# Optimization experiments

Hardware: AMD Instinct MI355X
Metric: run time of the kernel (lower is better)

The kernel has to match this reference:

```python
import jax, jax.numpy as jnp
import numpy as np

N = 50000        # nodes
E = 800000       # edges
IN_FEAT = 128
OUT_FEAT = 64
HEADS = 4
NUM_CLASSES = 40
NEG_SLOPE = 0.2  # DGL GATConv default


def setup_inputs() -> dict:
    key = jax.random.key(0)
    ks = jax.random.split(key, 12)
    x = jax.random.normal(ks[0], (N, IN_FEAT), dtype=jnp.float32)
    src = jax.random.randint(ks[1], (E,), 0, N, dtype=jnp.int32)
    dst = jax.random.randint(ks[2], (E,), 0, N, dtype=jnp.int32)
    # layer 1 params: fc W1 [in, H*D], attn_l/attn_r [H, D], bias [H*D]
    s1 = 1.0 / np.sqrt(IN_FEAT)
    W1 = jax.random.normal(ks[3], (IN_FEAT, HEADS * OUT_FEAT), dtype=jnp.float32) * s1
    al1 = jax.random.normal(ks[4], (HEADS, OUT_FEAT), dtype=jnp.float32) * 0.1
    ar1 = jax.random.normal(ks[5], (HEADS, OUT_FEAT), dtype=jnp.float32) * 0.1
    b1 = jnp.zeros((HEADS * OUT_FEAT,), dtype=jnp.float32)
    # layer 2 params: fc W2 [H*D, C], attn [1, C], bias [C]
    hid = HEADS * OUT_FEAT
    s2 = 1.0 / np.sqrt(hid)
    W2 = jax.random.normal(ks[6], (hid, NUM_CLASSES), dtype=jnp.float32) * s2
    al2 = jax.random.normal(ks[7], (1, NUM_CLASSES), dtype=jnp.float32) * 0.1
    ar2 = jax.random.normal(ks[8], (1, NUM_CLASSES), dtype=jnp.float32) * 0.1
    b2 = jnp.zeros((NUM_CLASSES,), dtype=jnp.float32)
    return {"x": x, "src": src, "dst": dst,
            "W1": W1, "al1": al1, "ar1": ar1, "b1": b1,
            "W2": W2, "al2": al2, "ar2": ar2, "b2": b2}


def gat_layer(x, W, al, ar, bias, src, dst, heads, out_feat):
    n = x.shape[0]
    h = (x @ W).reshape(n, heads, out_feat)            # [N,H,D]
    el = jnp.sum(h * al[None], axis=-1)                # [N,H]
    er = jnp.sum(h * ar[None], axis=-1)                # [N,H]
    e = el[src] + er[dst]                              # [E,H]
    e = jnp.where(e > 0, e, NEG_SLOPE * e)             # LeakyReLU
    # segment softmax over edges sharing the same destination
    emax = jax.ops.segment_max(e, dst, num_segments=n)           # [N,H]
    emax = jnp.where(jnp.isfinite(emax), emax, 0.0)              # isolated nodes
    ee = jnp.exp(e - emax[dst])                                  # [E,H]
    denom = jax.ops.segment_sum(ee, dst, num_segments=n)         # [N,H]
    denom = jnp.where(denom > 0, denom, 1.0)
    alpha = ee / denom[dst]                                      # [E,H]
    msg = h[src] * alpha[:, :, None]                             # [E,H,D]
    out = jax.ops.segment_sum(msg, dst, num_segments=n)          # [N,H,D]
    return out + bias.reshape(1, heads, out_feat)


def reference(x, src, dst, W1, al1, ar1, b1, W2, al2, ar2, b2):
    h = gat_layer(x, W1, al1, ar1, b1, src, dst, HEADS, OUT_FEAT)  # [N,H,D]
    h = h.reshape(h.shape[0], HEADS * OUT_FEAT)
    h = jax.nn.elu(h)
    h = gat_layer(h, W2, al2, ar2, b2, src, dst, 1, NUM_CLASSES)   # [N,1,C]
    return jnp.squeeze(h, axis=1)                                   # [N,C]
```

## Files before the change

### kernel.cpp

```cpp
#include <hip/hip_runtime.h>

#define NN 50000
#define NE 800000
#define HID 256
#define NCLS 40

typedef short bf16x8 __attribute__((ext_vector_type(8)));
typedef float f32x4 __attribute__((ext_vector_type(4)));

__device__ inline unsigned short f2bf(float f) {
    unsigned int u = __float_as_uint(f);
    return (unsigned short)((u + 0x7FFFu + ((u >> 16) & 1u)) >> 16);
}
__device__ inline unsigned int pack2bf(float a, float b) {
    return (unsigned int)f2bf(a) | ((unsigned int)f2bf(b) << 16);
}
__device__ inline float2 bf2x(unsigned int u) {
    return make_float2(__uint_as_float(u << 16), __uint_as_float(u & 0xFFFF0000u));
}

__global__ void k_count(const int* __restrict__ dst, int* __restrict__ counts) {
    int e = blockIdx.x * 256 + threadIdx.x;
    if (e < NE) atomicAdd(&counts[dst[e]], 1);
}

__global__ void k_scanA(const int* __restrict__ counts, int* __restrict__ indptr,
                        int* __restrict__ bsum) {
    __shared__ int sh[256];
    int t = threadIdx.x;
    int idx = blockIdx.x * 256 + t;
    int c = idx < NN ? counts[idx] : 0;
    sh[t] = c;
    __syncthreads();
    for (int off = 1; off < 256; off <<= 1) {
        int v = (t >= off) ? sh[t - off] : 0;
        __syncthreads();
        sh[t] += v;
        __syncthreads();
    }
    if (idx < NN) indptr[idx] = sh[t] - c;
    if (t == 255) bsum[blockIdx.x] = sh[255];
}

__global__ void k_scanB(int* __restrict__ bsum, int nb) {
    __shared__ int sh[256];
    int t = threadIdx.x;
    int c = t < nb ? bsum[t] : 0;
    sh[t] = c;
    __syncthreads();
    for (int off = 1; off < 256; off <<= 1) {
        int v = (t >= off) ? sh[t - off] : 0;
        __syncthreads();
        sh[t] += v;
        __syncthreads();
    }
    if (t < nb) bsum[t] = sh[t] - c;
}

__global__ void k_scanC(int* __restrict__ indptr, const int* __restrict__ bsum,
                        int* __restrict__ fill) {
    int idx = blockIdx.x * 256 + threadIdx.x;
    if (idx < NN) {
        indptr[idx] += bsum[idx >> 8];
        fill[idx] = 0;
    }
    if (idx == 0) indptr[NN] = NE;
}

__global__ void k_scatter(const int* __restrict__ src, const int* __restrict__ dst,
                          const int* __restrict__ indptr, int* __restrict__ fill,
                          int* __restrict__ srcs) {
    int e = blockIdx.x * 256 + threadIdx.x;
    if (e < NE) {
        int d = dst[e];
        int pos = atomicAdd(&fill[d], 1);
        srcs[indptr[d] + pos] = src[e];
    }
}

__global__ void k_prep(const float* __restrict__ W1, const float* __restrict__ al,
                       const float* __restrict__ ar, const float* __restrict__ W2,
                       float* __restrict__ wel, float* __restrict__ wer,
                       unsigned short* __restrict__ W1Tb,
                       unsigned short* __restrict__ W2Tb) {
    int gid = blockIdx.x * 256 + threadIdx.x;
    int nth = gridDim.x * 256;
    const int TOT = 512 + 32768 + 48 * 256;
    for (int i = gid; i < TOT; i += nth) {
        if (i < 512) {
            int k = i >> 2, h = i & 3;
            float a = 0.f, b = 0.f;
            for (int dd = 0; dd < 64; ++dd) {
                float w = W1[k * 256 + h * 64 + dd];
                a = fmaf(w, al[h * 64 + dd], a);
                b = fmaf(w, ar[h * 64 + dd], b);
            }
            wel[i] = a;
            wer[i] = b;
        } else if (i < 512 + 32768) {
            int j = i - 512;
            int col = j >> 7, k = j & 127;
            W1Tb[j] = f2bf(W1[k * 256 + col]);
        } else {
            int j = i - 512 - 32768;
            int col = j >> 8, kk = j & 255;
            W2Tb[j] = (col < NCLS) ? f2bf(W2[kk * 40 + col]) : (unsigned short)0;
        }
    }
}

__global__ void k_elr1x(const float* __restrict__ x, const float* __restrict__ wel,
                        const float* __restrict__ wer, float* __restrict__ el1,
                        float* __restrict__ er1, unsigned short* __restrict__ xb) {
    __shared__ float xs[64 * 129];
    __shared__ float wels[512], wers[512];
    int t = threadIdx.x;
    int n0 = blockIdx.x * 64;
    wels[t] = wel[t]; wels[256 + t] = wel[256 + t];
    wers[t] = wer[t]; wers[256 + t] = wer[256 + t];
    for (int i = 0; i < 8; ++i) {
        int f = i * 256 + t;
        int row = f >> 5;
        int col4 = (f & 31) * 4;
        float4 v = make_float4(0.f, 0.f, 0.f, 0.f);
        if (n0 + row < NN) v = ((const float4*)x)[(size_t)n0 * 32 + f];
        xs[row * 129 + col4 + 0] = v.x;
        xs[row * 129 + col4 + 1] = v.y;
        xs[row * 129 + col4 + 2] = v.z;
        xs[row * 129 + col4 + 3] = v.w;
    }
    __syncthreads();
    int node = t & 63;
    int h = t >> 6;
    float a = 0.f, b = 0.f;
    for (int k = 0; k < 128; ++k) {
        float xv = xs[node * 129 + k];
        a = fmaf(xv, wels[k * 4 + h], a);
        b = fmaf(xv, wers[k * 4 + h], b);
    }
    if (n0 + node < NN) {
        el1[(size_t)(n0 + node) * 4 + h] = a;
        er1[(size_t)(n0 + node) * 4 + h] = b;
    }
    for (int i = 0; i < 4; ++i) {
        int g = (i * 256 + t) * 8;
        int row = g >> 7, col = g & 127;
        if (n0 + row < NN) {
            ushort4 lo, hi;
            lo.x = f2bf(xs[row * 129 + col + 0]);
            lo.y = f2bf(xs[row * 129 + col + 1]);
            lo.z = f2bf(xs[row * 129 + col + 2]);
            lo.w = f2bf(xs[row * 129 + col + 3]);
            hi.x = f2bf(xs[row * 129 + col + 4]);
            hi.y = f2bf(xs[row * 129 + col + 5]);
            hi.z = f2bf(xs[row * 129 + col + 6]);
            hi.w = f2bf(xs[row * 129 + col + 7]);
            *(ushort4*)&xb[(size_t)(n0 + row) * 128 + col] = lo;
            *(ushort4*)&xb[(size_t)(n0 + row) * 128 + col + 4] = hi;
        }
    }
}

#define XG_STRIDE 260
__global__ void k_agg1m(const unsigned int* __restrict__ xb32,
                        const float* __restrict__ el1, const float* __restrict__ er1,
                        const int* __restrict__ indptr, const int* __restrict__ srcs,
                        const unsigned short* __restrict__ W1Tb,
                        const float* __restrict__ b1,
                        unsigned short* __restrict__ elu1) {
    __shared__ unsigned int xg[16 * XG_STRIDE];
    __shared__ int   si[4][64];
    __shared__ float4 sw[4][64];
    int t = threadIdx.x;
    int wv = t >> 6, l = t & 63;
    int n0 = blockIdx.x * 16;
    int d0 = n0 + wv * 4;
    int ip[5];
#pragma unroll
    for (int q = 0; q < 5; ++q) ip[q] = indptr[d0 + q];
    int s_next = 0;
    float4 ls_next = make_float4(0.f, 0.f, 0.f, 0.f);
    {
        int deg0 = ip[1] - ip[0];
        if (l < deg0) {
            s_next = srcs[ip[0] + l];
            ls_next = *(const float4*)&el1[(size_t)s_next * 4];
        }
    }
    for (int rr = 0; rr < 4; ++rr) {
        int d = d0 + rr;
        int beg = ip[rr], end = ip[rr + 1];
        int deg = end - beg;
        float4 rd = *(const float4*)&er1[(size_t)d * 4];
        int s_l = s_next;
        float4 ls = ls_next;
        float4 w = make_float4(0.f, 0.f, 0.f, 0.f);
        if (l < deg) {
            float e0 = ls.x + rd.x, e1 = ls.y + rd.y, e2 = ls.z + rd.z, e3 = ls.w + rd.w;
            e0 = e0 > 0.f ? e0 : 0.2f * e0;
            e1 = e1 > 0.f ? e1 : 0.2f * e1;
            e2 = e2 > 0.f ? e2 : 0.2f * e2;
            e3 = e3 > 0.f ? e3 : 0.2f * e3;
            w = make_float4(__expf(e0), __expf(e1), __expf(e2), __expf(e3));
        }
        si[wv][l] = s_l;
        sw[wv][l] = w;
        if (rr < 3) {
            int degn = ip[rr + 2] - ip[rr + 1];
            s_next = 0;
            ls_next = make_float4(0.f, 0.f, 0.f, 0.f);
            if (l < degn) {
                s_next = srcs[ip[rr + 1] + l];
                ls_next = *(const float4*)&el1[(size_t)s_next * 4];
            }
        }
        float2 a0 = {0.f, 0.f}, a1 = {0.f, 0.f}, a2 = {0.f, 0.f}, a3 = {0.f, 0.f};
        int dege = deg < 64 ? deg : 64;
        for (int e = 0; e < dege; e += 8) {
            int ixs[8];
            float4 wss[8];
            unsigned int us[8];
#pragma unroll
            for (int q = 0; q < 8; ++q) {
                ixs[q] = si[wv][e + q];
                wss[q] = sw[wv][e + q];
            }
#pragma unroll
            for (int q = 0; q < 8; ++q) us[q] = xb32[(size_t)ixs[q] * 64 + l];
#pragma unroll
            for (int q = 0; q < 8; ++q) {
                float2 xv = bf2x(us[q]);
                float4 wq = wss[q];
                a0.x = fmaf(wq.x, xv.x, a0.x); a0.y = fmaf(wq.x, xv.y, a0.y);
                a1.x = fmaf(wq.y, xv.x, a1.x); a1.y = fmaf(wq.y, xv.y, a1.y);
                a2.x = fmaf(wq.z, xv.x, a2.x); a2.y = fmaf(wq.z, xv.y, a2.y);
                a3.x = fmaf(wq.w, xv.x, a3.x); a3.y = fmaf(wq.w, xv.y, a3.y);
            }
        }
        float s0 = w.x, s1 = w.y, s2 = w.z, s3 = w.w;
        for (int j = beg + 64 + l; j < end; j += 64) {
            float4 lsx = *(const float4*)&el1[(size_t)srcs[j] * 4];
            float e0 = lsx.x + rd.x, e1 = lsx.y + rd.y, e2 = lsx.z + rd.z, e3 = lsx.w + rd.w;
            e0 = e0 > 0.f ? e0 : 0.2f * e0;
            e1 = e1 > 0.f ? e1 : 0.2f * e1;
            e2 = e2 > 0.f ? e2 : 0.2f * e2;
            e3 = e3 > 0.f ? e3 : 0.2f * e3;
            s0 += __expf(e0); s1 += __expf(e1); s2 += __expf(e2); s3 += __expf(e3);
        }
        for (int j = beg + 64; j < end; ++j) {
            int s = srcs[j];
            float4 lsx = *(const float4*)&el1[(size_t)s * 4];
            float e0 = lsx.x + rd.x, e1 = lsx.y + rd.y, e2 = lsx.z + rd.z, e3 = lsx.w + rd.w;
            e0 = e0 > 0.f ? e0 : 0.2f * e0;
            e1 = e1 > 0.f ? e1 : 0.2f * e1;
            e2 = e2 > 0.f ? e2 : 0.2f * e2;
            e3 = e3 > 0.f ? e3 : 0.2f * e3;
            float w0 = __expf(e0), w1 = __expf(e1), w2 = __expf(e2), w3 = __expf(e3);
            float2 xv = bf2x(xb32[(size_t)s * 64 + l]);
            a0.x = fmaf(w0, xv.x, a0.x); a0.y = fmaf(w0, xv.y, a0.y);
            a1.x = fmaf(w1, xv.x, a1.x); a1.y = fmaf(w1, xv.y, a1.y);
            a2.x = fmaf(w2, xv.x, a2.x); a2.y = fmaf(w2, xv.y, a2.y);
            a3.x = fmaf(w3, xv.x, a3.x); a3.y = fmaf(w3, xv.y, a3.y);
        }
#pragma unroll
        for (int off = 32; off > 0; off >>= 1) {
            s0 += __shfl_xor(s0, off);
            s1 += __shfl_xor(s1, off);
            s2 += __shfl_xor(s2, off);
            s3 += __shfl_xor(s3, off);
        }
        float i0 = s0 > 0.f ? 1.f / s0 : 0.f;
        float i1 = s1 > 0.f ? 1.f / s1 : 0.f;
        float i2 = s2 > 0.f ? 1.f / s2 : 0.f;
        float i3 = s3 > 0.f ? 1.f / s3 : 0.f;
        unsigned int* xgn = &xg[(wv * 4 + rr) * XG_STRIDE];
        xgn[0 * 64 + l] = pack2bf(a0.x * i0, a0.y * i0);
        xgn[1 * 64 + l] = pack2bf(a1.x * i1, a1.y * i1);
        xgn[2 * 64 + l] = pack2bf(a2.x * i2, a2.y * i2);
        xgn[3 * 64 + l] = pack2bf(a3.x * i3, a3.y * i3);
    }
    __syncthreads();
    int lrow = l & 15, lk = l >> 4;
    f32x4 acc[4] = {};
#pragma unroll
    for (int kt = 0; kt < 4; ++kt) {
        bf16x8 av = *(const bf16x8*)&xg[lrow * XG_STRIDE + wv * 64 + kt * 16 + lk * 4];
#pragma unroll
        for (int nt = 0; nt < 4; ++nt) {
            int col = wv * 64 + nt * 16 + lrow;
            bf16x8 bv = *(const bf16x8*)&W1Tb[(size_t)col * 128 + kt * 32 + lk * 8];
            acc[nt] = __builtin_amdgcn_mfma_f32_16x16x32_bf16(av, bv, acc[nt], 0, 0, 0);
        }
    }
#pragma unroll
    for (int nt = 0; nt < 4; ++nt) {
        int col = wv * 64 + nt * 16 + lrow;
        float bv1 = b1[col];
#pragma unroll
        for (int r = 0; r < 4; ++r) {
            int row = n0 + lk * 4 + r;
            float o = acc[nt][r] + bv1;
            o = o > 0.f ? o : (__expf(o) - 1.f);
            elu1[(size_t)row * 256 + col] = f2bf(o);
        }
    }
}

__global__ void k_mfma2(const unsigned short* __restrict__ elu1,
                        const unsigned short* __restrict__ W2Tb,
                        const float* __restrict__ al2, const float* __restrict__ ar2,
                        unsigned short* __restrict__ h2b, float* __restrict__ el2,
                        float* __restrict__ er2) {
    int t = threadIdx.x;
    int wv = t >> 6, l = t & 63;
    int lrow = l & 15, lk = l >> 4;
    int n0 = blockIdx.x * 64 + wv * 16;
    int arow = n0 + lrow;
    if (arow >= NN) arow = NN - 1;
    f32x4 acc[3] = {};
#pragma unroll
    for (int kt = 0; kt < 8; ++kt) {
        int kofs = kt * 32 + lk * 8;
        bf16x8 av = *(const bf16x8*)&elu1[(size_t)arow * 256 + kofs];
#pragma unroll
        for (int nt = 0; nt < 3; ++nt) {
            bf16x8 bv = *(const bf16x8*)&W2Tb[(size_t)(nt * 16 + lrow) * 256 + kofs];
            acc[nt] = __builtin_amdgcn_mfma_f32_16x16x32_bf16(av, bv, acc[nt], 0, 0, 0);
        }
    }
    float alc[3], arc[3];
#pragma unroll
    for (int nt = 0; nt < 3; ++nt) {
        int col = nt * 16 + lrow;
        alc[nt] = col < NCLS ? al2[col] : 0.f;
        arc[nt] = col < NCLS ? ar2[col] : 0.f;
    }
#pragma unroll
    for (int r = 0; r < 4; ++r) {
        int row = n0 + lk * 4 + r;
        float pa = 0.f, pb = 0.f;
#pragma unroll
        for (int nt = 0; nt < 3; ++nt) {
            float v = acc[nt][r];
            pa = fmaf(v, alc[nt], pa);
            pb = fmaf(v, arc[nt], pb);
            int col = nt * 16 + lrow;
            if (row < NN && col < NCLS) h2b[(size_t)row * NCLS + col] = f2bf(v);
        }
#pragma unroll
        for (int off = 1; off < 16; off <<= 1) {
            pa += __shfl_xor(pa, off);
            pb += __shfl_xor(pb, off);
        }
        if (lrow == 0 && row < NN) {
            el2[row] = pa;
            er2[row] = pb;
        }
    }
}

__global__ void k_agg2(const unsigned int* __restrict__ h2b32,
                       const float* __restrict__ el2,
                       const float* __restrict__ er2, const float* __restrict__ b2,
                       const int* __restrict__ indptr, const int* __restrict__ srcs,
                       float* __restrict__ out) {
    __shared__ int   si[4][64];
    __shared__ float sw[4][64];
    int t = threadIdx.x;
    int wv = t >> 6, l = t & 63;
    int d = blockIdx.x * 4 + wv;
    int beg = indptr[d], end = indptr[d + 1];
    int deg = end - beg;
    float rd = er2[d];
    int s_l = 0;
    float w = 0.f;
    if (l < deg) {
        s_l = srcs[beg + l];
        float e = el2[s_l] + rd;
        e = e > 0.f ? e : 0.2f * e;
        w = __expf(e);
    }
    si[wv][l] = s_l;
    sw[wv][l] = w;
    float den = w;
    for (int j = beg + 64 + l; j < end; j += 64) {
        float e = el2[srcs[j]] + rd;
        e = e > 0.f ? e : 0.2f * e;
        den += __expf(e);
    }
    int half = l >> 5, il = l & 31;
    bool act = il < 20;
    float2 acc = {0.f, 0.f};
    int dege = deg < 64 ? deg : 64;
    for (int e = 0; e < dege; e += 8) {
        int ixs[4];
        float ws_[4];
        unsigned int us[4];
#pragma unroll
        for (int q = 0; q < 4; ++q) {
            int idx = e + 2 * q + half;
            ixs[q] = si[wv][idx];
            ws_[q] = sw[wv][idx];
        }
#pragma unroll
        for (int q = 0; q < 4; ++q)
            us[q] = act ? h2b32[(size_t)ixs[q] * 20 + il] : 0u;
#pragma unroll
        for (int q = 0; q < 4; ++q) {
            float2 xv = bf2x(us[q]);
            acc.x = fmaf(ws_[q], xv.x, acc.x);
            acc.y = fmaf(ws_[q], xv.y, acc.y);
        }
    }
    for (int j = beg + 64; j < end; ++j) {
        int s = srcs[j];
        float e = el2[s] + rd;
        e = e > 0.f ? e : 0.2f * e;
        float ww = (half == 0) ? __expf(e) : 0.f;
        unsigned int u = act ? h2b32[(size_t)s * 20 + il] : 0u;
        float2 xv = bf2x(u);
        acc.x = fmaf(ww, xv.x, acc.x);
        acc.y = fmaf(ww, xv.y, acc.y);
    }
#pragma unroll
    for (int off = 32; off > 0; off >>= 1) den += __shfl_xor(den, off);
    float inv = den > 0.f ? 1.f / den : 0.f;
    acc.x += __shfl_xor(acc.x, 32);
    acc.y += __shfl_xor(acc.y, 32);
    if (half == 0 && act) {
        float2 bb = *(const float2*)&b2[2 * il];
        *(float2*)&out[(size_t)d * NCLS + 2 * il] =
            make_float2(fmaf(acc.x, inv, bb.x), fmaf(acc.y, inv, bb.y));
    }
}

extern "C" void kernel_launch(void* const* d_in, const int* in_sizes, int n_in,
                              void* d_out, int out_size, void* d_ws, size_t ws_size,
                              hipStream_t stream) {
    const float* x   = (const float*)d_in[0];
    const int*   src = (const int*)d_in[1];
    const int*   dst = (const int*)d_in[2];
    const float* W1  = (const float*)d_in[3];
    const float* al1 = (const float*)d_in[4];
    const float* ar1 = (const float*)d_in[5];
    const float* b1  = (const float*)d_in[6];
    const float* W2  = (const float*)d_in[7];
    const float* al2 = (const float*)d_in[8];
    const float* ar2 = (const float*)d_in[9];
    const float* b2  = (const float*)d_in[10];
    float* out = (float*)d_out;

    float* ws = (float*)d_ws;
    size_t off = 0;
    unsigned short* elu1  = (unsigned short*)(ws + off); off += (size_t)NN * 128;
    unsigned short* xb    = (unsigned short*)(ws + off); off += (size_t)NN * 64;
    unsigned short* h2b   = (unsigned short*)(ws + off); off += (size_t)NN * 20;
    float* el1  = ws + off; off += (size_t)NN * 4;
    float* er1  = ws + off; off += (size_t)NN * 4;
    float* el2  = ws + off; off += NN;
    float* er2  = ws + off; off += NN;
    float* wel  = ws + off; off += 512;
    float* wer  = ws + off; off += 512;
    unsigned short* w1tb = (unsigned short*)(ws + off); off += 16384;
    unsigned short* w2tb = (unsigned short*)(ws + off); off += 48 * 128;
    int* counts = (int*)(ws + off);
    int* indptr = counts + NN;
    int* fill   = indptr + NN + 1;
    int* srcs   = fill + NN;
    int* bsum   = srcs + NE;

    const int NB = (NN + 255) / 256;

    hipMemsetAsync(counts, 0, NN * sizeof(int), stream);

    k_count<<<(NE + 255) / 256, 256, 0, stream>>>(dst, counts);
    k_scanA<<<NB, 256, 0, stream>>>(counts, indptr, bsum);
    k_scanB<<<1, 256, 0, stream>>>(bsum, NB);
    k_scanC<<<NB, 256, 0, stream>>>(indptr, bsum, fill);
    k_scatter<<<(NE + 255) / 256, 256, 0, stream>>>(src, dst, indptr, fill, srcs);

    k_prep<<<48, 256, 0, stream>>>(W1, al1, ar1, W2, wel, wer, w1tb, w2tb);
    k_elr1x<<<(NN + 63) / 64, 256, 0, stream>>>(x, wel, wer, el1, er1, xb);
    k_agg1m<<<NN / 16, 256, 0, stream>>>((const unsigned int*)xb, el1, er1, indptr, srcs,
                                         w1tb, b1, elu1);

    k_mfma2<<<(NN + 63) / 64, 256, 0, stream>>>(elu1, w2tb, al2, ar2, h2b, el2, er2);
    k_agg2<<<NN / 4, 256, 0, stream>>>((const unsigned int*)h2b, el2, er2, b2,
                                       indptr, srcs, out);
}
```

Baseline: 236.2 us.

## Precompute layer-1 edge attention weights in CSR scatter and interleave two nodes per wave

Moves the layer-1 edge score computation (leaky ReLU and exp of el[src]+er[dst]) into the CSR scatter kernel, which now writes a per-edge float4 weight array alongside the sorted sources. The scatter launch is reordered to run after el1/er1 are computed. The aggregation kernel then reads those weights directly and processes two destination nodes per wave at once, interleaving their gathers to expose more memory-level parallelism. This trades a 12.8MB extra write and read of edge weights for removing the el1 gather and exp work in the aggregation, and it raises register and shared memory use.

```diff
diff --git a/kernel.cpp b/kernel.cpp
--- a/kernel.cpp
+++ b/kernel.cpp
@@ -67,14 +67,25 @@
     if (idx == 0) indptr[NN] = NE;
 }
 
-__global__ void k_scatter(const int* __restrict__ src, const int* __restrict__ dst,
-                          const int* __restrict__ indptr, int* __restrict__ fill,
-                          int* __restrict__ srcs) {
+__global__ void k_scatterw(const int* __restrict__ src, const int* __restrict__ dst,
+                           const int* __restrict__ indptr, int* __restrict__ fill,
+                           const float* __restrict__ el1, const float* __restrict__ er1,
+                           int* __restrict__ srcs, float4* __restrict__ w4) {
     int e = blockIdx.x * 256 + threadIdx.x;
     if (e < NE) {
         int d = dst[e];
+        int s = src[e];
         int pos = atomicAdd(&fill[d], 1);
-        srcs[indptr[d] + pos] = src[e];
+        int j = indptr[d] + pos;
+        srcs[j] = s;
+        float4 ls = *(const float4*)&el1[(size_t)s * 4];
+        float4 rd = *(const float4*)&er1[(size_t)d * 4];
+        float e0 = ls.x + rd.x, e1 = ls.y + rd.y, e2 = ls.z + rd.z, e3 = ls.w + rd.w;
+        e0 = e0 > 0.f ? e0 : 0.2f * e0;
+        e1 = e1 > 0.f ? e1 : 0.2f * e1;
+        e2 = e2 > 0.f ? e2 : 0.2f * e2;
+        e3 = e3 > 0.f ? e3 : 0.2f * e3;
+        w4[j] = make_float4(__expf(e0), __expf(e1), __expf(e2), __expf(e3));
     }
 }
 
@@ -162,15 +173,21 @@
 }
 
 #define XG_STRIDE 260
+#define FMA8(AC0, AC1, AC2, AC3, WQ, XV) \
+    AC0.x = fmaf(WQ.x, XV.x, AC0.x); AC0.y = fmaf(WQ.x, XV.y, AC0.y); \
+    AC1.x = fmaf(WQ.y, XV.x, AC1.x); AC1.y = fmaf(WQ.y, XV.y, AC1.y); \
+    AC2.x = fmaf(WQ.z, XV.x, AC2.x); AC2.y = fmaf(WQ.z, XV.y, AC2.y); \
+    AC3.x = fmaf(WQ.w, XV.x, AC3.x); AC3.y = fmaf(WQ.w, XV.y, AC3.y);
+
 __global__ void k_agg1m(const unsigned int* __restrict__ xb32,
-                        const float* __restrict__ el1, const float* __restrict__ er1,
+                        const float4* __restrict__ w4,
                         const int* __restrict__ indptr, const int* __restrict__ srcs,
                         const unsigned short* __restrict__ W1Tb,
                         const float* __restrict__ b1,
                         unsigned short* __restrict__ elu1) {
     __shared__ unsigned int xg[16 * XG_STRIDE];
-    __shared__ int   si[4][64];
-    __shared__ float4 sw[4][64];
+    __shared__ int   si[8][64];
+    __shared__ float4 sw[8][64];
     int t = threadIdx.x;
     int wv = t >> 6, l = t & 63;
     int n0 = blockIdx.x * 16;
@@ -178,106 +195,99 @@
     int ip[5];
 #pragma unroll
     for (int q = 0; q < 5; ++q) ip[q] = indptr[d0 + q];
-    int s_next = 0;
-    float4 ls_next = make_float4(0.f, 0.f, 0.f, 0.f);
-    {
-        int deg0 = ip[1] - ip[0];
-        if (l < deg0) {
-            s_next = srcs[ip[0] + l];
-            ls_next = *(const float4*)&el1[(size_t)s_next * 4];
-        }
-    }
-    for (int rr = 0; rr < 4; ++rr) {
-        int d = d0 + rr;
-        int beg = ip[rr], end = ip[rr + 1];
-        int deg = end - beg;
-        float4 rd = *(const float4*)&er1[(size_t)d * 4];
-        int s_l = s_next;
-        float4 ls = ls_next;
-        float4 w = make_float4(0.f, 0.f, 0.f, 0.f);
-        if (l < deg) {
-            float e0 = ls.x + rd.x, e1 = ls.y + rd.y, e2 = ls.z + rd.z, e3 = ls.w + rd.w;
-            e0 = e0 > 0.f ? e0 : 0.2f * e0;
-            e1 = e1 > 0.f ? e1 : 0.2f * e1;
-            e2 = e2 > 0.f ? e2 : 0.2f * e2;
-            e3 = e3 > 0.f ? e3 : 0.2f * e3;
-            w = make_float4(__expf(e0), __expf(e1), __expf(e2), __expf(e3));
-        }
-        si[wv][l] = s_l;
-        sw[wv][l] = w;
-        if (rr < 3) {
-            int degn = ip[rr + 2] - ip[rr + 1];
-            s_next = 0;
-            ls_next = make_float4(0.f, 0.f, 0.f, 0.f);
-            if (l < degn) {
-                s_next = srcs[ip[rr + 1] + l];
-                ls_next = *(const float4*)&el1[(size_t)s_next * 4];
+    int w2 = wv * 2;
+#pragma unroll
+    for (int p = 0; p < 2; ++p) {
+        int begA = ip[2 * p + 0], endA = ip[2 * p + 1];
+        int begB = ip[2 * p + 1], endB = ip[2 * p + 2];
+        int degA = endA - begA, degB = endB - begB;
+        int sA = 0, sB = 0;
+        float4 wA = make_float4(0.f, 0.f, 0.f, 0.f);
+        float4 wB = make_float4(0.f, 0.f, 0.f, 0.f);
+        if (l < degA) { sA = srcs[begA + l]; wA = w4[begA + l]; }
+        if (l < degB) { sB = srcs[begB + l]; wB = w4[begB + l]; }
+        si[w2 + 0][l] = sA; sw[w2 + 0][l] = wA;
+        si[w2 + 1][l] = sB; sw[w2 + 1][l] = wB;
+        float2 aA0 = {0,0}, aA1 = {0,0}, aA2 = {0,0}, aA3 = {0,0};
+        float2 aB0 = {0,0}, aB1 = {0,0}, aB2 = {0,0}, aB3 = {0,0};
+        int capA = degA < 64 ? degA : 64;
+        int capB = degB < 64 ? degB : 64;
+        int mcap = capA > capB ? capA : capB;
+        for (int e = 0; e < mcap; e += 8) {
+            unsigned int uA[8], uB[8];
+            bool doA = e < capA, doB = e < capB;
+            if (doA) {
+#pragma unroll
+                for (int q = 0; q < 8; ++q)
+                    uA[q] = xb32[(size_t)si[w2][e + q] * 64 + l];
             }
-        }
-        float2 a0 = {0.f, 0.f}, a1 = {0.f, 0.f}, a2 = {0.f, 0.f}, a3 = {0.f, 0.f};
-        int dege = deg < 64 ? deg : 64;
-        for (int e = 0; e < dege; e += 8) {
-            int ixs[8];
-            float4 wss[8];
-            unsigned int us[8];
-#pragma unroll
-            for (int q = 0; q < 8; ++q) {
-                ixs[q] = si[wv][e + q];
-                wss[q] = sw[wv][e + q];
+            if (doB) {
+#pragma unroll
+                for (int q = 0; q < 8; ++q)
+                    uB[q] = xb32[(size_t)si[w2 + 1][e + q] * 64 + l];
             }
-#pragma unroll
-            for (int q = 0; q < 8; ++q) us[q] = xb32[(size_t)ixs[q] * 64 + l];
-#pragma unroll
-            for (int q = 0; q < 8; ++q) {
-                float2 xv = bf2x(us[q]);
-                float4 wq = wss[q];
-                a0.x = fmaf(wq.x, xv.x, a0.x); a0.y = fmaf(wq.x, xv.y, a0.y);
-                a1.x = fmaf(wq.y, xv.x, a1.x); a1.y = fmaf(wq.y, xv.y, a1.y);
-                a2.x = fmaf(wq.z, xv.x, a2.x); a2.y = fmaf(wq.z, xv.y, a2.y);
-                a3.x = fmaf(wq.w, xv.x, a3.x); a3.y = fmaf(wq.w, xv.y, a3.y);
+            if (doA) {
+#pragma unroll
+                for (int q = 0; q < 8; ++q) {
+                    float4 wq = sw[w2][e + q];
+                    float2 xv = bf2x(uA[q]);
+                    FMA8(aA0, aA1, aA2, aA3, wq, xv)
+                }
             }
-        }
-        float s0 = w.x, s1 = w.y, s2 = w.z, s3 = w.w;
-        for (int j = beg + 64 + l; j < end; j += 64) {
-            float4 lsx = *(const float4*)&el1[(size_t)srcs[j] * 4];
-            float e0 = lsx.x + rd.x, e1 = lsx.y + rd.y, e2 = lsx.z + rd.z, e3 = lsx.w + rd.w;
-            e0 = e0 > 0.f ? e0 : 0.2f * e0;
-            e1 = e1 > 0.f ? e1 : 0.2f * e1;
-            e2 = e2 > 0.f ? e2 : 0.2f * e2;
-            e3 = e3 > 0.f ? e3 : 0.2f * e3;
-            s0 += __expf(e0); s1 += __expf(e1); s2 += __expf(e2); s3 += __expf(e3);
-        }
-        for (int j = beg + 64; j < end; ++j) {
-            int s = srcs[j];
-            float4 lsx = *(const float4*)&el1[(size_t)s * 4];
-            float e0 = lsx.x + rd.x, e1 = lsx.y + rd.y, e2 = lsx.z + rd.z, e3 = lsx.w + rd.w;
-            e0 = e0 > 0.f ? e0 : 0.2f * e0;
-            e1 = e1 > 0.f ? e1 : 0.2f * e1;
-            e2 = e2 > 0.f ? e2 : 0.2f * e2;
-            e3 = e3 > 0.f ? e3 : 0.2f * e3;
-            float w0 = __expf(e0), w1 = __expf(e1), w2 = __expf(e2), w3 = __expf(e3);
-            float2 xv = bf2x(xb32[(size_t)s * 64 + l]);
-            a0.x = fmaf(w0, xv.x, a0.x); a0.y = fmaf(w0, xv.y, a0.y);
-            a1.x = fmaf(w1, xv.x, a1.x); a1.y = fmaf(w1, xv.y, a1.y);
-            a2.x = fmaf(w2, xv.x, a2.x); a2.y = fmaf(w2, xv.y, a2.y);
-            a3.x = fmaf(w3, xv.x, a3.x); a3.y = fmaf(w3, xv.y, a3.y);
+            if (doB) {
+#pragma unroll
+                for (int q = 0; q < 8; ++q) {
+                    float4 wq = sw[w2 + 1][e + q];
+                    float2 xv = bf2x(uB[q]);
+                    FMA8(aB0, aB1, aB2, aB3, wq, xv)
+                }
+            }
+        }
+        for (int j = begA + 64; j < endA; ++j) {
+            float4 wq = w4[j];
+            float2 xv = bf2x(xb32[(size_t)srcs[j] * 64 + l]);
+            FMA8(aA0, aA1, aA2, aA3, wq, xv)
+        }
+        for (int j = begB + 64; j < endB; ++j) {
+            float4 wq = w4[j];
+            float2 xv = bf2x(xb32[(size_t)srcs[j] * 64 + l]);
+            FMA8(aB0, aB1, aB2, aB3, wq, xv)
+        }
+        float dA0 = wA.x, dA1 = wA.y, dA2 = wA.z, dA3 = wA.w;
+        float dB0 = wB.x, dB1 = wB.y, dB2 = wB.z, dB3 = wB.w;
+        for (int j = begA + 64 + l; j < endA; j += 64) {
+            float4 wt = w4[j];
+            dA0 += wt.x; dA1 += wt.y; dA2 += wt.z; dA3 += wt.w;
+        }
+        for (int j = begB + 64 + l; j < endB; j += 64) {
+            float4 wt = w4[j];
+            dB0 += wt.x; dB1 += wt.y; dB2 += wt.z; dB3 += wt.w;
         }
 #pragma unroll
         for (int off = 32; off > 0; off >>= 1) {
-            s0 += __shfl_xor(s0, off);
-            s1 += __shfl_xor(s1, off);
-            s2 += __shfl_xor(s2, off);
-            s3 += __shfl_xor(s3, off);
-        }
-        float i0 = s0 > 0.f ? 1.f / s0 : 0.f;
-        float i1 = s1 > 0.f ? 1.f / s1 : 0.f;
-        float i2 = s2 > 0.f ? 1.f / s2 : 0.f;
-        float i3 = s3 > 0.f ? 1.f / s3 : 0.f;
-        unsigned int* xgn = &xg[(wv * 4 + rr) * XG_STRIDE];
-        xgn[0 * 64 + l] = pack2bf(a0.x * i0, a0.y * i0);
-        xgn[1 * 64 + l] = pack2bf(a1.x * i1, a1.y * i1);
-        xgn[2 * 64 + l] = pack2bf(a2.x * i2, a2.y * i2);
-        xgn[3 * 64 + l] = pack2bf(a3.x * i3, a3.y * i3);
+            dA0 += __shfl_xor(dA0, off); dA1 += __shfl_xor(dA1, off);
+            dA2 += __shfl_xor(dA2, off); dA3 += __shfl_xor(dA3, off);
+            dB0 += __shfl_xor(dB0, off); dB1 += __shfl_xor(dB1, off);
+            dB2 += __shfl_xor(dB2, off); dB3 += __shfl_xor(dB3, off);
+        }
+        float iA0 = dA0 > 0.f ? 1.f / dA0 : 0.f;
+        float iA1 = dA1 > 0.f ? 1.f / dA1 : 0.f;
+        float iA2 = dA2 > 0.f ? 1.f / dA2 : 0.f;
+        float iA3 = dA3 > 0.f ? 1.f / dA3 : 0.f;
+        float iB0 = dB0 > 0.f ? 1.f / dB0 : 0.f;
+        float iB1 = dB1 > 0.f ? 1.f / dB1 : 0.f;
+        float iB2 = dB2 > 0.f ? 1.f / dB2 : 0.f;
+        float iB3 = dB3 > 0.f ? 1.f / dB3 : 0.f;
+        unsigned int* xgA = &xg[(wv * 4 + 2 * p + 0) * XG_STRIDE];
+        xgA[0 * 64 + l] = pack2bf(aA0.x * iA0, aA0.y * iA0);
+        xgA[1 * 64 + l] = pack2bf(aA1.x * iA1, aA1.y * iA1);
+        xgA[2 * 64 + l] = pack2bf(aA2.x * iA2, aA2.y * iA2);
+        xgA[3 * 64 + l] = pack2bf(aA3.x * iA3, aA3.y * iA3);
+        unsigned int* xgB = &xg[(wv * 4 + 2 * p + 1) * XG_STRIDE];
+        xgB[0 * 64 + l] = pack2bf(aB0.x * iB0, aB0.y * iB0);
+        xgB[1 * 64 + l] = pack2bf(aB1.x * iB1, aB1.y * iB1);
+        xgB[2 * 64 + l] = pack2bf(aB2.x * iB2, aB2.y * iB2);
+        xgB[3 * 64 + l] = pack2bf(aB3.x * iB3, aB3.y * iB3);
     }
     __syncthreads();
     int lrow = l & 15, lk = l >> 4;
@@ -463,6 +473,7 @@
     float* wer  = ws + off; off += 512;
     unsigned short* w1tb = (unsigned short*)(ws + off); off += 16384;
     unsigned short* w2tb = (unsigned short*)(ws + off); off += 48 * 128;
+    float* w4   = ws + off; off += (size_t)NE * 4;
     int* counts = (int*)(ws + off);
     int* indptr = counts + NN;
     int* fill   = indptr + NN + 1;
@@ -477,12 +488,13 @@
     k_scanA<<<NB, 256, 0, stream>>>(counts, indptr, bsum);
     k_scanB<<<1, 256, 0, stream>>>(bsum, NB);
     k_scanC<<<NB, 256, 0, stream>>>(indptr, bsum, fill);
-    k_scatter<<<(NE + 255) / 256, 256, 0, stream>>>(src, dst, indptr, fill, srcs);
 
     k_prep<<<48, 256, 0, stream>>>(W1, al1, ar1, W2, wel, wer, w1tb, w2tb);
     k_elr1x<<<(NN + 63) / 64, 256, 0, stream>>>(x, wel, wer, el1, er1, xb);
-    k_agg1m<<<NN / 16, 256, 0, stream>>>((const unsigned int*)xb, el1, er1, indptr, srcs,
-                                         w1tb, b1, elu1);
+    k_scatterw<<<(NE + 255) / 256, 256, 0, stream>>>(src, dst, indptr, fill,
+                                                     el1, er1, srcs, (float4*)w4);
+    k_agg1m<<<NN / 16, 256, 0, stream>>>((const unsigned int*)xb, (const float4*)w4,
+                                         indptr, srcs, w1tb, b1, elu1);
 
     k_mfma2<<<(NN + 63) / 64, 256, 0, stream>>>(elu1, w2tb, al2, ar2, h2b, el2, er2);
     k_agg2<<<NN / 4, 256, 0, stream>>>((const unsigned int*)h2b, el2, er2, b2,
```

Result: faster. 215.4 us (-8.8%).
